# Performance work log

Measured on AMD Instinct MI355X. Metric: run time of the kernel, lower is better.

## Reference

```python
import jax, jax.numpy as jnp
import numpy as np


def _degree_norms(src, dst, n_nodes):
    ones = jnp.ones(src.shape[0], dtype=jnp.float32)
    deg_out = jax.ops.segment_sum(ones, src, num_segments=n_nodes)
    deg_in = jax.ops.segment_sum(ones, dst, num_segments=n_nodes)
    # DGL GraphConv clamps degrees to min 1 before pow(-0.5)
    norm_src = jnp.power(jnp.maximum(deg_out, 1.0), -0.5)
    norm_dst = jnp.power(jnp.maximum(deg_in, 1.0), -0.5)
    return norm_src, norm_dst


def _graph_conv(h, src, dst, norm_src, norm_dst, W, b, activation):
    n_nodes = h.shape[0]
    # norm='both': scale source features, project, aggregate, scale dest
    x = h * norm_src[:, None]
    x = x @ W                                   # [N, out]
    m = x[src]                                  # gather  [E, out]
    agg = jax.ops.segment_sum(m, dst, num_segments=n_nodes)  # scatter-add [N, out]
    out = agg * norm_dst[:, None] + b
    if activation is not None:
        out = activation(out)
    return out


def setup_inputs() -> dict:
    key = jax.random.key(0)
    k = jax.random.split(key, 6)
    N, E, F, D = 100000, 1600000, 128, 128
    feature = jax.random.normal(k[0], (N, F), dtype=jnp.float32)
    src = jax.random.randint(k[1], (E,), 0, N, dtype=jnp.int32)
    dst = jax.random.randint(k[2], (E,), 0, N, dtype=jnp.int32)
    W1 = jax.random.normal(k[3], (F, D), dtype=jnp.float32) / np.sqrt(F)
    b1 = jnp.zeros((D,), dtype=jnp.float32)
    W2 = jax.random.normal(k[4], (D, D), dtype=jnp.float32) / np.sqrt(D)
    b2 = jnp.zeros((D,), dtype=jnp.float32)
    return {"feature": feature, "src": src, "dst": dst,
            "W1": W1, "b1": b1, "W2": W2, "b2": b2}


def reference(feature, src, dst, W1, b1, W2, b2):
    n_nodes = feature.shape[0]
    norm_src, norm_dst = _degree_norms(src, dst, n_nodes)
    # layer 0: relu; layer 1 (last): no activation
    h = _graph_conv(feature, src, dst, norm_src, norm_dst, W1, b1, jax.nn.relu)
    h = _graph_conv(h, src, dst, norm_src, norm_dst, W2, b2, None)
    return h
```

## Files before the change

### kernel.cpp

```cpp
#include <hip/hip_runtime.h>


#define RS_LOG 10
#define RS (1 << RS_LOG)
#define EPB 4096

typedef short bf16x8 __attribute__((ext_vector_type(8)));
typedef float f32x4 __attribute__((ext_vector_type(4)));

__device__ __forceinline__ unsigned short rne_bf16(float v) {
  unsigned u = __float_as_uint(v);
  return (unsigned short)((u + 0x7FFF + ((u >> 16) & 1)) >> 16);
}

__device__ __forceinline__ void load_lds16(const void* g, void* l) {
  __builtin_amdgcn_global_load_lds((const __attribute__((address_space(1))) unsigned*)g,
                                   (__attribute__((address_space(3))) unsigned*)l, 16, 0, 0);
}

__global__ void build_graph(const int* __restrict__ src, const int* __restrict__ dst,
                            int* __restrict__ cursor, int* __restrict__ deg_out,
                            int* __restrict__ padded, int E, int CAP) {
  int e = blockIdx.x * blockDim.x + threadIdx.x;
  if (e < E) {
    int s = src[e];
    int d = dst[e];
    atomicAdd(&deg_out[s], 1);
    int pos = atomicAdd(&cursor[d], 1);
    if (pos < CAP) padded[(size_t)d * CAP + pos] = s;
  }
}

__global__ __launch_bounds__(256) void partition_edges(
    const int* __restrict__ src, const int* __restrict__ dst, int* __restrict__ g_cnt,
    int* __restrict__ part_dst, unsigned short* __restrict__ part_src, int E, int NR, int CAPR) {
  __shared__ int cntD[256], locD[256], baseD[256];
  __shared__ int cntS[256], locS[256], baseS[256];
  __shared__ unsigned stageD[EPB];
  __shared__ unsigned short stageS[EPB];
  __shared__ unsigned char rngD[EPB], rngS[EPB];
  int t = threadIdx.x;
  int e0 = blockIdx.x * EPB;
  int e1 = min(e0 + EPB, E);
  int nE = e1 - e0;
  cntD[t] = 0;
  cntS[t] = 0;
  __syncthreads();
  for (int e = e0 + t; e < e1; e += 256) {
    atomicAdd(&cntD[dst[e] >> RS_LOG], 1);
    atomicAdd(&cntS[src[e] >> RS_LOG], 1);
  }
  __syncthreads();
  locD[t] = cntD[t];
  locS[t] = cntS[t];
  __syncthreads();
  for (int ofs = 1; ofs < 256; ofs <<= 1) {
    int aD = (t >= ofs) ? locD[t - ofs] : 0;
    int aS = (t >= ofs) ? locS[t - ofs] : 0;
    __syncthreads();
    locD[t] += aD;
    locS[t] += aS;
    __syncthreads();
  }
  int exD = locD[t] - cntD[t];
  int exS = locS[t] - cntS[t];
  __syncthreads();
  locD[t] = exD;
  locS[t] = exS;
  if (t < NR) {
    baseD[t] = atomicAdd(&g_cnt[t * 16], cntD[t]);
    baseS[t] = atomicAdd(&g_cnt[(NR + t) * 16], cntS[t]);
  }
  cntD[t] = 0;
  cntS[t] = 0;
  __syncthreads();
  for (int e = e0 + t; e < e1; e += 256) {
    int s = src[e];
    int d = dst[e];
    int rd = d >> RS_LOG;
    int rs = s >> RS_LOG;
    int pd = locD[rd] + atomicAdd(&cntD[rd], 1);
    stageD[pd] = ((unsigned)(d & (RS - 1)) << 17) | (unsigned)s;
    rngD[pd] = (unsigned char)rd;
    int ps = locS[rs] + atomicAdd(&cntS[rs], 1);
    stageS[ps] = (unsigned short)(s & (RS - 1));
    rngS[ps] = (unsigned char)rs;
  }
  __syncthreads();
  for (int i = t; i < nE; i += 256) {
    int r = rngD[i];
    int pos = baseD[r] + (i - locD[r]);
    if (pos < CAPR) part_dst[(size_t)r * CAPR + pos] = stageD[i];
    int r2 = rngS[i];
    int pos2 = baseS[r2] + (i - locS[r2]);
    if (pos2 < CAPR) part_src[(size_t)r2 * CAPR + pos2] = stageS[i];
  }
}

__global__ __launch_bounds__(512) void build_structures(
    const int* __restrict__ g_cnt, const int* __restrict__ part_dst,
    const unsigned short* __restrict__ part_src, int* __restrict__ padded,
    int* __restrict__ deg_in, int* __restrict__ deg_out, int N, int NR, int CAPR, int CAP) {
  __shared__ int cur[RS];
  int t = threadIdx.x;
  int b = blockIdx.x;
  for (int i = t; i < RS; i += 512) cur[i] = 0;
  __syncthreads();
  if (b < NR) {
    int cnt = min(g_cnt[b * 16], CAPR);
    const int* p = part_dst + (size_t)b * CAPR;
    for (int i = t; i < cnt; i += 512) {
      int v = p[i];
      int dlow = v >> 17;
      int s = v & 0x1FFFF;
      int pos = atomicAdd(&cur[dlow], 1);
      if (pos < CAP) padded[((size_t)((b << RS_LOG) + dlow)) * CAP + pos] = s;
    }
    __syncthreads();
    int nbase = b << RS_LOG;
    for (int i = t; i < RS; i += 512) {
      int node = nbase + i;
      if (node < N) deg_in[node] = cur[i];
    }
  } else {
    int r = b - NR;
    int cnt = min(g_cnt[(NR + r) * 16], CAPR);
    const unsigned short* p = part_src + (size_t)r * CAPR;
    for (int i = t; i < cnt; i += 512) atomicAdd(&cur[p[i]], 1);
    __syncthreads();
    int nbase = r << RS_LOG;
    for (int i = t; i < RS; i += 512) {
      int node = nbase + i;
      if (node < N) deg_out[node] = cur[i];
    }
  }
}

__global__ void compute_norms(const int* __restrict__ deg_out, const int* __restrict__ deg_in,
                              float* __restrict__ norm_src, float* __restrict__ norm_dst, int N) {
  int i = blockIdx.x * blockDim.x + threadIdx.x;
  if (i < N) {
    norm_src[i] = rsqrtf((float)max(deg_out[i], 1));
    norm_dst[i] = rsqrtf((float)max(deg_in[i], 1));
  }
}

__global__ __launch_bounds__(256) void prep_w_frag(const float* __restrict__ W,
                                                   unsigned short* __restrict__ Wfrag) {
  int idx = blockIdx.x * 256 + threadIdx.x;
  int j = idx & 7;
  int l = (idx >> 3) & 63;
  int chunk = idx >> 9;
  int nr = chunk >> 2;
  int s = chunk & 3;
  int col = nr * 16 + (l & 15);
  int k = s * 32 + (l >> 4) * 8 + j;
  float w = W[k * 128 + col];
  unsigned short h = rne_bf16(w);
  float hf = __uint_as_float((unsigned)h << 16);
  unsigned short lo = rne_bf16(w - hf);
  Wfrag[((chunk * 2 + 0) * 64 + l) * 8 + j] = h;
  Wfrag[((chunk * 2 + 1) * 64 + l) * 8 + j] = lo;
}

__global__ __launch_bounds__(512, 1) void gemm_mfma_p(const float* __restrict__ X,
                                                      const unsigned short* __restrict__ Wfrag,
                                                      const float* __restrict__ norm,
                                                      unsigned short* __restrict__ Ybf, int N) {
  extern __shared__ unsigned char smem[];
  unsigned char* Wl = smem;
  unsigned char* Xa = smem + 65536;
  unsigned char* Xb = smem + 98304;
  int t = threadIdx.x;
  int lane = t & 63;
  int wv = t >> 6;

#pragma unroll
  for (int j = 0; j < 8; j++) {
    int d = j * 8192 + t * 16;
    load_lds16((const unsigned char*)Wfrag + d, Wl + d);
  }

  auto stage = [&](unsigned char* dstb, int tr0) {
    long vb = ((long)N - tr0) * 512;
    const unsigned char* xbase = (const unsigned char*)X + (size_t)tr0 * 512;
#pragma unroll
    for (int j = 0; j < 4; j++) {
      int d = j * 8192 + t * 16;
      int off = d ^ (((d >> 9) & 7) << 4);
      long o = off;
      if (o >= vb) o = 0;
      load_lds16(xbase + o, dstb + d);
    }
  };

  int tile = blockIdx.x;
  stage(Xa, tile * 64);
  asm volatile("s_waitcnt vmcnt(0)" ::: "memory");
  __syncthreads();

  int c = lane & 15;
  int kgrp = lane >> 4;
  int g = wv & 3;
  int nb = (wv >> 2) * 4;
  unsigned char* Xcur = Xa;
  unsigned char* Xnxt = Xb;

  for (; tile * 64 < N; tile += gridDim.x) {
    int tr0 = tile * 64;
    int nxt_r0 = (tile + gridDim.x) * 64;
    if (nxt_r0 < N) stage(Xnxt, nxt_r0);

    int rloc = g * 16 + c;
    int rowA = tr0 + rloc;
    float nn = (rowA < N) ? norm[rowA] : 0.f;
    f32x4 acc[4];
#pragma unroll
    for (int nr = 0; nr < 4; nr++) acc[nr] = (f32x4){0.f, 0.f, 0.f, 0.f};

#pragma unroll
    for (int s = 0; s < 4; s++) {
      int byteA = rloc * 512 + (s * 32 + kgrp * 8) * 4;
      int a0 = byteA ^ ((rloc & 7) << 4);
      float4 xa = *(const float4*)(Xcur + a0);
      float4 xb2 = *(const float4*)(Xcur + (a0 ^ 16));
      bf16x8 ah, al;
      {
        float v[8] = {xa.x, xa.y, xa.z, xa.w, xb2.x, xb2.y, xb2.z, xb2.w};
#pragma unroll
        for (int j = 0; j < 8; j++) {
          float a = v[j] * nn;
          unsigned short h = rne_bf16(a);
          ah[j] = (short)h;
          al[j] = (short)rne_bf16(a - __uint_as_float((unsigned)h << 16));
        }
      }
#pragma unroll
      for (int nr = 0; nr < 4; nr++) {
        int chunk = (nb + nr) * 4 + s;
        bf16x8 bh = *(const bf16x8*)(Wl + (chunk * 2 + 0) * 1024 + lane * 16);
        bf16x8 bl = *(const bf16x8*)(Wl + (chunk * 2 + 1) * 1024 + lane * 16);
        acc[nr] = __builtin_amdgcn_mfma_f32_16x16x32_bf16(ah, bh, acc[nr], 0, 0, 0);
        acc[nr] = __builtin_amdgcn_mfma_f32_16x16x32_bf16(al, bh, acc[nr], 0, 0, 0);
        acc[nr] = __builtin_amdgcn_mfma_f32_16x16x32_bf16(ah, bl, acc[nr], 0, 0, 0);
      }
    }

    asm volatile("s_waitcnt vmcnt(0)" ::: "memory");
    __syncthreads();

    int rb = tr0 + g * 16 + kgrp * 4;
#pragma unroll
    for (int q = 0; q < 4; q++) {
      int row = rb + q;
      if (row < N) {
        unsigned short* yo = Ybf + (size_t)row * 128 + nb * 16 + c;
#pragma unroll
        for (int nr = 0; nr < 4; nr++) yo[nr * 16] = rne_bf16(acc[nr][q]);
      }
    }
    unsigned char* tmp = Xcur;
    Xcur = Xnxt;
    Xnxt = tmp;
  }
}

__global__ __launch_bounds__(256) void spmm_bf(const unsigned* __restrict__ Ybf,
                                               const int* __restrict__ padded,
                                               const int* __restrict__ deg_in,
                                               const float* __restrict__ norm_dst,
                                               const float* __restrict__ bias,
                                               float* __restrict__ out, int N, int CAP,
                                               int do_relu) {
  int t = threadIdx.x;
  int lane = t & 63;
  int wv = t >> 6;
  int v = blockIdx.x * 4 + wv;
  if (v >= N) return;
  int cnt = min(deg_in[v], CAP);
  int sidx = (lane < cnt) ? padded[(size_t)v * CAP + lane] : 0;
  float ax = 0.f, ay = 0.f;
  int i = 0;
  for (; i + 4 <= cnt; i += 4) {
    int s0 = __builtin_amdgcn_readlane(sidx, i);
    int s1 = __builtin_amdgcn_readlane(sidx, i + 1);
    int s2 = __builtin_amdgcn_readlane(sidx, i + 2);
    int s3 = __builtin_amdgcn_readlane(sidx, i + 3);
    unsigned w0 = Ybf[(size_t)s0 * 64 + lane];
    unsigned w1 = Ybf[(size_t)s1 * 64 + lane];
    unsigned w2 = Ybf[(size_t)s2 * 64 + lane];
    unsigned w3 = Ybf[(size_t)s3 * 64 + lane];
    ax += __uint_as_float(w0 << 16) + __uint_as_float(w1 << 16) +
          __uint_as_float(w2 << 16) + __uint_as_float(w3 << 16);
    ay += __uint_as_float(w0 & 0xFFFF0000u) + __uint_as_float(w1 & 0xFFFF0000u) +
          __uint_as_float(w2 & 0xFFFF0000u) + __uint_as_float(w3 & 0xFFFF0000u);
  }
  for (; i < cnt; i++) {
    int s = __builtin_amdgcn_readlane(sidx, i);
    unsigned w = Ybf[(size_t)s * 64 + lane];
    ax += __uint_as_float(w << 16);
    ay += __uint_as_float(w & 0xFFFF0000u);
  }
  float nd = norm_dst[v];
  float2 b = ((const float2*)bias)[lane];
  float2 r;
  r.x = ax * nd + b.x;
  r.y = ay * nd + b.y;
  if (do_relu) {
    r.x = fmaxf(r.x, 0.f);
    r.y = fmaxf(r.y, 0.f);
  }
  ((float2*)out)[(size_t)v * 64 + lane] = r;
}

extern "C" void kernel_launch(void* const* d_in, const int* in_sizes, int n_in,
                              void* d_out, int out_size, void* d_ws, size_t ws_size,
                              hipStream_t stream) {
  const float* feature = (const float*)d_in[0];
  const int* src = (const int*)d_in[1];
  const int* dst = (const int*)d_in[2];
  const float* W1 = (const float*)d_in[3];
  const float* b1 = (const float*)d_in[4];
  const float* W2 = (const float*)d_in[5];
  const float* b2 = (const float*)d_in[6];
  float* out = (float*)d_out;

  const int F = 128;
  int N = in_sizes[0] / F;
  int E = in_sizes[1];
  (void)n_in;
  (void)out_size;

  char* ws = (char*)d_ws;
  size_t off = 0;
  auto alloc = [&](size_t bytes) -> char* {
    char* p = ws + off;
    off = (off + bytes + 255) & ~(size_t)255;
    return p;
  };
  float* h_buf = (float*)alloc((size_t)N * F * 4);
  int* degs = (int*)alloc((size_t)2 * N * 4);
  int* deg_in_ = degs;
  int* deg_out_ = degs + N;
  float* norm_src = (float*)alloc((size_t)N * 4);
  float* norm_dst = (float*)alloc((size_t)N * 4);
  unsigned short* wfrag1 = (unsigned short*)alloc(32768 * 2);
  unsigned short* wfrag2 = (unsigned short*)alloc(32768 * 2);

  int NR = (N + RS - 1) >> RS_LOG;
  int CAPR = (E + NR - 1) / NR + 4096;
  CAPR = (CAPR + 31) & ~31;
  size_t part_bytes =
      (size_t)NR * CAPR * 4 + (size_t)NR * CAPR * 2 + (size_t)2 * NR * 16 * 4 + 1024;
  size_t avail = (ws_size > off) ? ws_size - off : 0;

  int CAP;
  bool partition_ok = (N <= 131072) && (NR <= 255);
  bool use_part;
  if (partition_ok && avail >= (size_t)N * 64 * 4 + part_bytes) {
    CAP = 64;
    use_part = true;
  } else if (partition_ok && avail >= (size_t)N * 48 * 4 + part_bytes) {
    CAP = 48;
    use_part = true;
  } else if (avail >= (size_t)N * 64 * 4 + (size_t)N * 4 + 256) {
    CAP = 64;
    use_part = false;
  } else if (avail >= (size_t)N * 48 * 4 + (size_t)N * 4 + 256) {
    CAP = 48;
    use_part = false;
  } else {
    CAP = 32;
    use_part = false;
  }
  int* padded = (int*)alloc((size_t)N * CAP * 4);

  prep_w_frag<<<64, 256, 0, stream>>>(W1, wfrag1);
  prep_w_frag<<<64, 256, 0, stream>>>(W2, wfrag2);

  if (use_part) {
    int* part_dst = (int*)alloc((size_t)NR * CAPR * 4);
    unsigned short* part_src = (unsigned short*)alloc((size_t)NR * CAPR * 2);
    int* g_cnt = (int*)alloc((size_t)2 * NR * 16 * 4);
    int NB = (E + EPB - 1) / EPB;
    hipMemsetAsync(g_cnt, 0, (size_t)2 * NR * 16 * 4, stream);
    partition_edges<<<NB, 256, 0, stream>>>(src, dst, g_cnt, part_dst, part_src, E, NR, CAPR);
    build_structures<<<2 * NR, 512, 0, stream>>>(g_cnt, part_dst, part_src, padded, deg_in_,
                                                 deg_out_, N, NR, CAPR, CAP);
  } else {
    int* cursor = (int*)alloc((size_t)N * 4);
    hipMemsetAsync(degs, 0, (size_t)2 * N * 4, stream);
    build_graph<<<(E + 255) / 256, 256, 0, stream>>>(src, dst, deg_in_, deg_out_, padded, E, CAP);
    (void)cursor;
  }
  compute_norms<<<(N + 255) / 256, 256, 0, stream>>>(deg_out_, deg_in_, norm_src, norm_dst, N);

  unsigned short* ybf1 = (unsigned short*)d_out;
  unsigned short* ybf2;
  float* final_target;
  bool need_copy;
  size_t ybf_bytes = (size_t)N * 128 * 2;
  if (ws_size > off && ws_size - off >= ybf_bytes + 256) {
    ybf2 = (unsigned short*)alloc(ybf_bytes);
    final_target = out;
    need_copy = false;
  } else {
    ybf2 = (unsigned short*)d_out;
    final_target = h_buf;
    need_copy = true;
  }

  int ntiles = (N + 63) / 64;
  int gb = ntiles < 256 ? ntiles : 256;
  gemm_mfma_p<<<gb, 512, 131072, stream>>>(feature, wfrag1, norm_src, ybf1, N);
  spmm_bf<<<(N + 3) / 4, 256, 0, stream>>>((const unsigned*)ybf1, padded, deg_in_, norm_dst, b1,
                                           h_buf, N, CAP, 1);
  gemm_mfma_p<<<gb, 512, 131072, stream>>>(h_buf, wfrag2, norm_src, ybf2, N);
  spmm_bf<<<(N + 3) / 4, 256, 0, stream>>>((const unsigned*)ybf2, padded, deg_in_, norm_dst, b2,
                                           final_target, N, CAP, 0);
  if (need_copy) {
    hipMemcpyAsync(out, h_buf, (size_t)N * F * 4, hipMemcpyDeviceToDevice, stream);
  }
}
```

Before: 333.6 us.

## Slice projected features into column planes and gather per slice in SpMM

The GEMM now writes bf16 output in eight column-sliced planes of 16 features each. The SpMM is rewritten so each block handles one slice for 16 destination nodes, with lanes split into 4 node groups of 16 columns, and neighbour indices are broadcast via ds_bpermute. The intent is to keep each plane's working set small enough to stay cache-resident during the random gather. It trades this for 2-byte per-lane loads, repeated index reads per slice, and smaller, less coalesced stores.

```diff
diff --git a/kernel.cpp b/kernel.cpp
--- a/kernel.cpp
+++ b/kernel.cpp
@@ -166,7 +166,7 @@
 __global__ __launch_bounds__(512, 1) void gemm_mfma_p(const float* __restrict__ X,
                                                       const unsigned short* __restrict__ Wfrag,
                                                       const float* __restrict__ norm,
-                                                      unsigned short* __restrict__ Ybf, int N) {
+                                                      unsigned short* __restrict__ Yp, int N) {
   extern __shared__ unsigned char smem[];
   unsigned char* Wl = smem;
   unsigned char* Xa = smem + 65536;
@@ -254,9 +254,10 @@
     for (int q = 0; q < 4; q++) {
       int row = rb + q;
       if (row < N) {
-        unsigned short* yo = Ybf + (size_t)row * 128 + nb * 16 + c;
-#pragma unroll
-        for (int nr = 0; nr < 4; nr++) yo[nr * 16] = rne_bf16(acc[nr][q]);
+#pragma unroll
+        for (int nr = 0; nr < 4; nr++) {
+          Yp[(size_t)(nb + nr) * N * 16 + (size_t)row * 16 + c] = rne_bf16(acc[nr][q]);
+        }
       }
     }
     unsigned char* tmp = Xcur;
@@ -265,52 +266,60 @@
   }
 }
 
-__global__ __launch_bounds__(256) void spmm_bf(const unsigned* __restrict__ Ybf,
-                                               const int* __restrict__ padded,
-                                               const int* __restrict__ deg_in,
-                                               const float* __restrict__ norm_dst,
-                                               const float* __restrict__ bias,
-                                               float* __restrict__ out, int N, int CAP,
-                                               int do_relu) {
+__global__ __launch_bounds__(256) void spmm_sliced(const unsigned short* __restrict__ Yp,
+                                                   const int* __restrict__ padded,
+                                                   const int* __restrict__ deg_in,
+                                                   const float* __restrict__ norm_dst,
+                                                   const float* __restrict__ bias,
+                                                   float* __restrict__ out, int N, int CAP,
+                                                   int do_relu) {
   int t = threadIdx.x;
   int lane = t & 63;
   int wv = t >> 6;
-  int v = blockIdx.x * 4 + wv;
-  if (v >= N) return;
-  int cnt = min(deg_in[v], CAP);
-  int sidx = (lane < cnt) ? padded[(size_t)v * CAP + lane] : 0;
-  float ax = 0.f, ay = 0.f;
-  int i = 0;
-  for (; i + 4 <= cnt; i += 4) {
-    int s0 = __builtin_amdgcn_readlane(sidx, i);
-    int s1 = __builtin_amdgcn_readlane(sidx, i + 1);
-    int s2 = __builtin_amdgcn_readlane(sidx, i + 2);
-    int s3 = __builtin_amdgcn_readlane(sidx, i + 3);
-    unsigned w0 = Ybf[(size_t)s0 * 64 + lane];
-    unsigned w1 = Ybf[(size_t)s1 * 64 + lane];
-    unsigned w2 = Ybf[(size_t)s2 * 64 + lane];
-    unsigned w3 = Ybf[(size_t)s3 * 64 + lane];
-    ax += __uint_as_float(w0 << 16) + __uint_as_float(w1 << 16) +
-          __uint_as_float(w2 << 16) + __uint_as_float(w3 << 16);
-    ay += __uint_as_float(w0 & 0xFFFF0000u) + __uint_as_float(w1 & 0xFFFF0000u) +
-          __uint_as_float(w2 & 0xFFFF0000u) + __uint_as_float(w3 & 0xFFFF0000u);
-  }
-  for (; i < cnt; i++) {
-    int s = __builtin_amdgcn_readlane(sidx, i);
-    unsigned w = Ybf[(size_t)s * 64 + lane];
-    ax += __uint_as_float(w << 16);
-    ay += __uint_as_float(w & 0xFFFF0000u);
-  }
-  float nd = norm_dst[v];
-  float2 b = ((const float2*)bias)[lane];
-  float2 r;
-  r.x = ax * nd + b.x;
-  r.y = ay * nd + b.y;
-  if (do_relu) {
-    r.x = fmaxf(r.x, 0.f);
-    r.y = fmaxf(r.y, 0.f);
-  }
-  ((float2*)out)[(size_t)v * 64 + lane] = r;
+  int slice = blockIdx.x & 7;
+  int chunk = blockIdx.x >> 3;
+  int g = lane >> 4;
+  int il = lane & 15;
+  int v = chunk * 16 + wv * 4 + g;
+  bool okv = v < N;
+  int cnt = okv ? min(deg_in[v], CAP) : 0;
+  int mc = max(cnt, __shfl_xor(cnt, 16));
+  mc = max(mc, __shfl_xor(mc, 32));
+
+  const unsigned short* plane = Yp + (size_t)slice * N * 16;
+  float acc = 0.f;
+  for (int r = 0; r * 16 < mc; r++) {
+    int slot = r * 16 + il;
+    int sidx = (okv && slot < cnt) ? padded[(size_t)v * CAP + slot] : 0;
+    int lim = min(mc - r * 16, 16);
+    for (int i0 = 0; i0 < lim; i0 += 8) {
+      int s_[8];
+      int act_[8];
+#pragma unroll
+      for (int u = 0; u < 8; u++) {
+        int i = i0 + u;
+        int s = __builtin_amdgcn_ds_bpermute((g * 16 + (i & 15)) * 4, sidx);
+        int a = (r * 16 + i) < cnt;
+        s_[u] = a ? s : 0;
+        act_[u] = a;
+      }
+      float w_[8];
+#pragma unroll
+      for (int u = 0; u < 8; u++) {
+        unsigned w = (unsigned)plane[(size_t)s_[u] * 16 + il];
+        w_[u] = __uint_as_float(w << 16);
+      }
+#pragma unroll
+      for (int u = 0; u < 8; u++) acc += act_[u] ? w_[u] : 0.f;
+    }
+  }
+  if (okv) {
+    float nd = norm_dst[v];
+    float bb = bias[slice * 16 + il];
+    float rres = acc * nd + bb;
+    if (do_relu) rres = fmaxf(rres, 0.f);
+    out[(size_t)v * 128 + slice * 16 + il] = rres;
+  }
 }
 
 extern "C" void kernel_launch(void* const* d_in, const int* in_sizes, int n_in,
@@ -412,12 +421,13 @@
 
   int ntiles = (N + 63) / 64;
   int gb = ntiles < 256 ? ntiles : 256;
+  int schunks = (N + 15) / 16;
   gemm_mfma_p<<<gb, 512, 131072, stream>>>(feature, wfrag1, norm_src, ybf1, N);
-  spmm_bf<<<(N + 3) / 4, 256, 0, stream>>>((const unsigned*)ybf1, padded, deg_in_, norm_dst, b1,
-                                           h_buf, N, CAP, 1);
+  spmm_sliced<<<schunks * 8, 256, 0, stream>>>(ybf1, padded, deg_in_, norm_dst, b1, h_buf, N,
+                                               CAP, 1);
   gemm_mfma_p<<<gb, 512, 131072, stream>>>(h_buf, wfrag2, norm_src, ybf2, N);
-  spmm_bf<<<(N + 3) / 4, 256, 0, stream>>>((const unsigned*)ybf2, padded, deg_in_, norm_dst, b2,
-                                           final_target, N, CAP, 0);
+  spmm_sliced<<<schunks * 8, 256, 0, stream>>>(ybf2, padded, deg_in_, norm_dst, b2, final_target,
+                                               N, CAP, 0);
   if (need_copy) {
     hipMemcpyAsync(out, h_buf, (size_t)N * F * 4, hipMemcpyDeviceToDevice, stream);
   }
```

Result: slower. 421.7 us (+26.4%).
